# Kernel tuning notes

Measured on AMD Instinct MI355X. Metric: run time of the kernel, lower is better.

Reference implementation:

```python
import jax, jax.numpy as jnp
import numpy as np

SEQ, D_IN, D_OUT = 8192, 768, 768

def setup_inputs() -> dict:
    key = jax.random.key(0)
    k1, k2, k3, k4 = jax.random.split(key, 4)
    scale = 1.0 / np.sqrt(D_IN)
    return {
        "x": jax.random.normal(k1, (SEQ, D_IN), dtype=jnp.float32),
        "w_q": jax.random.normal(k2, (D_OUT, D_IN), dtype=jnp.float32) * scale,
        "w_k": jax.random.normal(k3, (D_OUT, D_IN), dtype=jnp.float32) * scale,
        "w_v": jax.random.normal(k4, (D_OUT, D_IN), dtype=jnp.float32) * scale,
    }

def reference(x, w_q, w_k, w_v):
    # torch Linear: y = x @ W.T (no bias since qkv_bias=False)
    q = x @ w_q.T  # [S, D]
    k = x @ w_k.T  # [S, D]
    v = x @ w_v.T  # [S, D]
    scores = (q @ k.T) / jnp.sqrt(jnp.asarray(k.shape[-1], x.dtype))  # [S, S]
    attn = jax.nn.softmax(scores, axis=-1)
    return attn @ v  # [S, D]
```

## Files before the change

kernel.cpp:

```cpp
#include <hip/hip_runtime.h>

#define SEQ 8192
#define DIM 768

typedef __attribute__((ext_vector_type(8))) short s16x8;
typedef __attribute__((ext_vector_type(4))) float f32x4;

__device__ __forceinline__ unsigned short f2bf(float f) {
  union { float f; unsigned u; } v; v.f = f;
  unsigned r = v.u + 0x7FFFu + ((v.u >> 16) & 1u);
  return (unsigned short)(r >> 16);
}

__device__ __forceinline__ float bf2f(unsigned short s) {
  union { unsigned u; float f; } v; v.u = ((unsigned)s) << 16;
  return v.f;
}

__device__ __forceinline__ void gll16(const void* gsrc, void* ldst) {
  __builtin_amdgcn_global_load_lds(
      (__attribute__((address_space(1))) unsigned int*)gsrc,
      (__attribute__((address_space(3))) unsigned int*)ldst, 16, 0, 0);
}

#define XN4 (SEQ * DIM / 4)
#define WN4 (DIM * DIM / 4)

__global__ void cast_all_kernel(const float* __restrict__ x, const float* __restrict__ wq,
                                const float* __restrict__ wk, const float* __restrict__ wv,
                                unsigned short* __restrict__ dx, unsigned short* __restrict__ dq,
                                unsigned short* __restrict__ dk, unsigned short* __restrict__ dv) {
  int i = blockIdx.x * blockDim.x + threadIdx.x;
  const float* s;
  unsigned short* d;
  int off;
  if (i < XN4) {
    s = x; d = dx; off = i;
  } else {
    int j = i - XN4;
    int wi = j / WN4;
    off = j - wi * WN4;
    s = (wi == 0) ? wq : ((wi == 1) ? wk : wv);
    d = (wi == 0) ? dq : ((wi == 1) ? dk : dv);
  }
  float4 v = ((const float4*)s)[off];
  ushort4 r; r.x = f2bf(v.x); r.y = f2bf(v.y); r.z = f2bf(v.z); r.w = f2bf(v.w);
  ((ushort4*)d)[off] = r;
}

__global__ __launch_bounds__(256, 2)
void proj_kernel(const unsigned short* __restrict__ X,
                 const unsigned short* __restrict__ Wq,
                 const unsigned short* __restrict__ Wk,
                 const unsigned short* __restrict__ Wv,
                 unsigned short* __restrict__ Qb,
                 unsigned short* __restrict__ Kb,
                 unsigned short* __restrict__ Vtb) {
  __shared__ __align__(16) char lds[65536];
  const int tid = threadIdx.x;
  const int lane = tid & 63, wv = tid >> 6;
  const int l15 = lane & 15, l4 = lane >> 4;
  const int mt = blockIdx.x, nt = blockIdx.y, z = blockIdx.z;
  const unsigned short* W = (z == 0) ? Wq : ((z == 1) ? Wk : Wv);

  f32x4 acc[4][4];
#pragma unroll
  for (int i = 0; i < 4; ++i)
#pragma unroll
    for (int j = 0; j < 4; ++j) acc[i][j] = f32x4{0.f, 0.f, 0.f, 0.f};

  auto stage = [&](int kk) {
    char* At = lds + (kk & 1) * 32768;
    char* Bt = At + 16384;
    const int d0 = kk * 64;
#pragma unroll
    for (int i = 0; i < 4; ++i) {
      int s = i * 256 + tid;
      int row = s >> 3, c = (s & 7) ^ (row & 7);
      gll16(X + (long)(mt * 128 + row) * DIM + d0 + c * 8, At + i * 4096 + (wv << 10));
      gll16(W + (long)(nt * 128 + row) * DIM + d0 + c * 8, Bt + i * 4096 + (wv << 10));
    }
  };

  stage(0);
#pragma unroll 1
  for (int kk = 0; kk < 12; ++kk) {
    __syncthreads();
    if (kk + 1 < 12) stage(kk + 1);
    const char* At = lds + (kk & 1) * 32768;
    const char* Bt = At + 16384;
#pragma unroll
    for (int ks = 0; ks < 2; ++ks) {
      const int c = ks * 4 + l4;
      s16x8 a[4], b[4];
#pragma unroll
      for (int mi = 0; mi < 4; ++mi) {
        int row = (wv & 1) * 64 + mi * 16 + l15;
        a[mi] = *(const s16x8*)(At + row * 128 + ((c ^ (row & 7)) << 4));
      }
#pragma unroll
      for (int ni = 0; ni < 4; ++ni) {
        int row = (wv >> 1) * 64 + ni * 16 + l15;
        b[ni] = *(const s16x8*)(Bt + row * 128 + ((c ^ (row & 7)) << 4));
      }
#pragma unroll
      for (int mi = 0; mi < 4; ++mi)
#pragma unroll
        for (int ni = 0; ni < 4; ++ni)
          acc[mi][ni] = __builtin_amdgcn_mfma_f32_16x16x32_bf16(a[mi], b[ni], acc[mi][ni], 0, 0, 0);
    }
  }

#pragma unroll
  for (int mi = 0; mi < 4; ++mi)
#pragma unroll
    for (int ni = 0; ni < 4; ++ni) {
      int row0 = mt * 128 + (wv & 1) * 64 + mi * 16 + l4 * 4;
      int col = nt * 128 + (wv >> 1) * 64 + ni * 16 + l15;
      if (z == 2) {
        ushort4 r;
        r.x = f2bf(acc[mi][ni][0]); r.y = f2bf(acc[mi][ni][1]);
        r.z = f2bf(acc[mi][ni][2]); r.w = f2bf(acc[mi][ni][3]);
        *(ushort4*)(Vtb + (long)(row0 >> 5) * (DIM * 32) + col * 32 + (row0 & 31)) = r;
      } else {
        unsigned short* dst = (z == 0) ? Qb : Kb;
#pragma unroll
        for (int g = 0; g < 4; ++g)
          dst[(long)(row0 + g) * DIM + col] = f2bf(acc[mi][ni][g]);
      }
    }
}

#define SCALE_LOG2E 0.05205878f

__global__ __launch_bounds__(512, 2)
void flash_kernel(const unsigned short* __restrict__ Q,
                  const unsigned short* __restrict__ K,
                  const unsigned short* __restrict__ V,
                  unsigned short* __restrict__ partp,
                  float* __restrict__ outf,
                  float* __restrict__ lout,
                  int kv_len, int norm_out) {
  __shared__ __align__(16) char lds[131072];
  char* Pl = lds + 98304;
  float* l_part = (float*)lds;

  const int tid = threadIdx.x;
  const int lane = tid & 63, wv = tid >> 6;
  const int l15 = lane & 15, l4 = lane >> 4;
  const int qtile = blockIdx.x, split = blockIdx.y;
  const long kv0 = (long)split * kv_len;
  const long qrow0 = (long)qtile * 64;
  const int R = wv & 1;
  const int C = wv >> 1;

  f32x4 acc_o[4][6];
  float acc_lp[8];
#pragma unroll
  for (int i = 0; i < 4; ++i)
#pragma unroll
    for (int j = 0; j < 6; ++j) acc_o[i][j] = f32x4{0.f, 0.f, 0.f, 0.f};
#pragma unroll
  for (int i = 0; i < 8; ++i) acc_lp[i] = 0.f;

  const int niter = kv_len >> 8;

  auto vchunk = [&](int par, int j) -> char* {
    int base = par ? ((j < 5) ? 40960 + j * 8192 : 90112)
                   : ((j < 5) ? j * 8192 : 81920);
    return lds + base;
  };

  auto stageQK = [&](int r, long kbase) {
    char* Qc = lds + (r & 1) * 40960;
    char* Kc = Qc + 8192;
    const int d0 = r * 64;
    {
      int s = tid;
      int row = s >> 3, c = (s & 7) ^ (row & 7);
      gll16(Q + (qrow0 + row) * DIM + d0 + c * 8, Qc + (wv << 10));
    }
#pragma unroll
    for (int i = 0; i < 4; ++i) {
      int s = i * 512 + tid;
      int row = s >> 3, c = (s & 7) ^ (row & 7);
      gll16(K + (kbase + row) * DIM + d0 + c * 8, Kc + i * 8192 + (wv << 10));
    }
  };

  auto stagePV = [&](int v, long kblk0) {
    const int par = v & 1;
    const long blkbase = (kblk0 + v) * (long)(DIM * 32);
    int s = wv * 64 + lane;
    int rp = s >> 3, p3 = s & 7;
    int orig = p3 ^ (rp & 7);
    int vr_in = rp * 2 + (orig >> 2);
    int k4 = orig & 3;
#pragma unroll
    for (int i = 0; i < 6; ++i)
      gll16(V + blkbase + (long)(i * 128 + vr_in) * 32 + k4 * 8, vchunk(par, i) + (wv << 10));
  };

  stageQK(0, kv0);
#pragma unroll 1
  for (int it = 0; it < niter; ++it) {
    const long kb = kv0 + (long)it * 256;
    const long kblk0 = kb >> 5;

    f32x4 acc_s[2][4];
#pragma unroll
    for (int a = 0; a < 2; ++a)
#pragma unroll
      for (int b = 0; b < 4; ++b) acc_s[a][b] = f32x4{0.f, 0.f, 0.f, 0.f};

#pragma unroll 1
    for (int r = 0; r < 12; ++r) {
      __syncthreads();
      if (r + 1 < 12) stageQK(r + 1, kb);
      else stagePV(0, kblk0);
      const char* Qc = lds + (r & 1) * 40960;
      const char* Kc = Qc + 8192;
#pragma unroll
      for (int ks = 0; ks < 2; ++ks) {
        const int c = ks * 4 + l4;
        s16x8 af[2], bk[4];
#pragma unroll
        for (int rt = 0; rt < 2; ++rt) {
          int row = R * 32 + rt * 16 + l15;
          af[rt] = *(const s16x8*)(Qc + row * 128 + ((c ^ (row & 7)) << 4));
        }
#pragma unroll
        for (int ct = 0; ct < 4; ++ct) {
          int kr = C * 64 + ct * 16 + l15;
          bk[ct] = *(const s16x8*)(Kc + kr * 128 + ((c ^ (kr & 7)) << 4));
        }
        __builtin_amdgcn_s_setprio(1);
#pragma unroll
        for (int rt = 0; rt < 2; ++rt)
#pragma unroll
          for (int ct = 0; ct < 4; ++ct)
            acc_s[rt][ct] = __builtin_amdgcn_mfma_f32_16x16x32_bf16(af[rt], bk[ct], acc_s[rt][ct], 0, 0, 0);
        __builtin_amdgcn_s_setprio(0);
      }
    }

#pragma unroll
    for (int rt = 0; rt < 2; ++rt)
#pragma unroll
      for (int ct = 0; ct < 4; ++ct)
#pragma unroll
        for (int g = 0; g < 4; ++g) {
          float p = exp2f(acc_s[rt][ct][g] * SCALE_LOG2E);
          acc_lp[rt * 4 + g] += p;
          int row = R * 32 + rt * 16 + l4 * 4 + g;
          int col = C * 64 + ct * 16 + l15;
          int off = row * 512 + ((((col >> 3) ^ (row & 7))) << 4) + ((col & 7) << 1);
          *(unsigned short*)(Pl + off) = f2bf(p);
        }

#pragma unroll 1
    for (int v = 0; v < 8; ++v) {
      __syncthreads();
      if (v + 1 < 8) stagePV(v + 1, kblk0);
      else if (it + 1 < niter) stageQK(0, kb + 256);
      const int par = v & 1;
      s16x8 pa[4];
      const int ck = v * 4 + l4;
#pragma unroll
      for (int rs = 0; rs < 4; ++rs) {
        int row = rs * 16 + l15;
        int pc = (ck & ~7) | ((ck & 7) ^ (row & 7));
        pa[rs] = *(const s16x8*)(Pl + row * 512 + (pc << 4));
      }
      const int vr_l = wv * 16 + l15;
      const int rp = vr_l >> 1;
      const int p3 = (((l15 & 1) << 2) | l4) ^ (rp & 7);
#pragma unroll
      for (int cc = 0; cc < 3; ++cc)
#pragma unroll
        for (int t = 0; t < 2; ++t) {
          const char* vcb = vchunk(par, cc * 2 + t);
          s16x8 vb = *(const s16x8*)(vcb + rp * 128 + (p3 << 4));
          __builtin_amdgcn_s_setprio(1);
#pragma unroll
          for (int rs = 0; rs < 4; ++rs)
            acc_o[rs][cc * 2 + t] =
                __builtin_amdgcn_mfma_f32_16x16x32_bf16(pa[rs], vb, acc_o[rs][cc * 2 + t], 0, 0, 0);
          __builtin_amdgcn_s_setprio(0);
        }
    }
  }

#pragma unroll
  for (int i = 0; i < 8; ++i) {
    float v = acc_lp[i];
    v += __shfl_xor(v, 1); v += __shfl_xor(v, 2);
    v += __shfl_xor(v, 4); v += __shfl_xor(v, 8);
    acc_lp[i] = v;
  }
  __syncthreads();
  if (l15 == 0) {
#pragma unroll
    for (int rt = 0; rt < 2; ++rt)
#pragma unroll
      for (int g = 0; g < 4; ++g)
        l_part[C * 64 + R * 32 + rt * 16 + l4 * 4 + g] = acc_lp[rt * 4 + g];
  }
  __syncthreads();

  if (!norm_out) {
    if (tid < 64)
      lout[(long)split * SEQ + qrow0 + tid] =
          l_part[tid] + l_part[64 + tid] + l_part[128 + tid] + l_part[192 + tid];
#pragma unroll
    for (int rt = 0; rt < 4; ++rt) {
      int row = rt * 16 + l4 * 4;
#pragma unroll
      for (int j = 0; j < 6; ++j) {
        int cc = j >> 1, t = j & 1;
        int col = (cc * 16 + wv + 8 * t) * 16 + l15;
#pragma unroll
        for (int g = 0; g < 4; ++g)
          partp[(long)split * SEQ * DIM + (qrow0 + row + g) * DIM + col] = f2bf(acc_o[rt][j][g]);
      }
    }
  } else {
    float linv[4][4];
#pragma unroll
    for (int rt = 0; rt < 4; ++rt)
#pragma unroll
      for (int g = 0; g < 4; ++g) {
        int row = rt * 16 + l4 * 4 + g;
        linv[rt][g] = 1.0f / (l_part[row] + l_part[64 + row] + l_part[128 + row] + l_part[192 + row]);
      }
#pragma unroll
    for (int rt = 0; rt < 4; ++rt) {
      int row = rt * 16 + l4 * 4;
#pragma unroll
      for (int j = 0; j < 6; ++j) {
        int cc = j >> 1, t = j & 1;
        int col = (cc * 16 + wv + 8 * t) * 16 + l15;
#pragma unroll
        for (int g = 0; g < 4; ++g)
          outf[(qrow0 + row + g) * DIM + col] = acc_o[rt][j][g] * linv[rt][g];
      }
    }
  }
}

__global__ void combine_kernel(const unsigned short* __restrict__ part,
                               const float* __restrict__ lsum,
                               float* __restrict__ out, int n4) {
  int i = blockIdx.x * blockDim.x + threadIdx.x;
  if (i >= n4) return;
  int row = (i * 4) / DIM;
  ushort4 p0 = ((const ushort4*)part)[i];
  ushort4 p1 = ((const ushort4*)(part + (long)SEQ * DIM))[i];
  float inv = 1.0f / (lsum[row] + lsum[SEQ + row]);
  float4 o;
  o.x = (bf2f(p0.x) + bf2f(p1.x)) * inv;
  o.y = (bf2f(p0.y) + bf2f(p1.y)) * inv;
  o.z = (bf2f(p0.z) + bf2f(p1.z)) * inv;
  o.w = (bf2f(p0.w) + bf2f(p1.w)) * inv;
  ((float4*)out)[i] = o;
}

extern "C" void kernel_launch(void* const* d_in, const int* in_sizes, int n_in,
                              void* d_out, int out_size, void* d_ws, size_t ws_size,
                              hipStream_t stream) {
  const float* x = (const float*)d_in[0];
  const float* wq = (const float*)d_in[1];
  const float* wk = (const float*)d_in[2];
  const float* wv = (const float*)d_in[3];
  float* out = (float*)d_out;
  char* ws = (char*)d_ws;

  const size_t o_xbf = 0;
  const size_t o_wq = o_xbf + (size_t)SEQ * DIM * 2;
  const size_t o_wk = o_wq + (size_t)DIM * DIM * 2;
  const size_t o_wv = o_wk + (size_t)DIM * DIM * 2;
  const size_t o_q = o_wv + (size_t)DIM * DIM * 2;
  const size_t o_k = o_q + (size_t)SEQ * DIM * 2;
  const size_t o_vt = o_k + (size_t)SEQ * DIM * 2;
  const size_t o_part = o_vt + (size_t)SEQ * DIM * 2;
  const size_t o_l = o_part + (size_t)2 * SEQ * DIM * 2;
  const size_t total_g2 = o_l + (size_t)2 * SEQ * 4;

  unsigned short* Xbf = (unsigned short*)(ws + o_xbf);
  unsigned short* Wqb = (unsigned short*)(ws + o_wq);
  unsigned short* Wkb = (unsigned short*)(ws + o_wk);
  unsigned short* Wvb = (unsigned short*)(ws + o_wv);
  unsigned short* Qb = (unsigned short*)(ws + o_q);
  unsigned short* Kb = (unsigned short*)(ws + o_k);
  unsigned short* Vtb = (unsigned short*)(ws + o_vt);
  unsigned short* part = (unsigned short*)(ws + o_part);
  float* lbuf = (float*)(ws + o_l);

  const int G = (ws_size >= total_g2) ? 2 : 1;

  cast_all_kernel<<<7872, 256, 0, stream>>>(x, wq, wk, wv, Xbf, Wqb, Wkb, Wvb);
  proj_kernel<<<dim3(64, 6, 3), 256, 0, stream>>>(Xbf, Wqb, Wkb, Wvb, Qb, Kb, Vtb);
  if (G == 2) {
    flash_kernel<<<dim3(128, 2), 512, 0, stream>>>(Qb, Kb, Vtb, part, nullptr, lbuf, SEQ / 2, 0);
    combine_kernel<<<6144, 256, 0, stream>>>(part, lbuf, out, SEQ * DIM / 4);
  } else {
    flash_kernel<<<dim3(128, 1), 512, 0, stream>>>(Qb, Kb, Vtb, nullptr, out, nullptr, SEQ, 1);
  }
}
```

Baseline: 315.9 us.

## Load V fragments directly from global into registers, removing PV LDS staging

The PV phase no longer stages V blocks through LDS with async global-to-LDS copies and per-chunk barriers. Each wave now loads its V fragments straight into registers from the pre-tiled V layout, double-buffered across the eight chunks. The next Q/K stage is prefetched at the end of the QK loop instead. This removes eight barriers per iteration and shrinks LDS, at the cost of more vector registers and exposed global load latency inside the MFMA loop.

```diff
diff --git a/kernel.cpp b/kernel.cpp
--- a/kernel.cpp
+++ b/kernel.cpp
@@ -133,6 +133,35 @@
 
 #define SCALE_LOG2E 0.05205878f
 
+#define LOADVB(arr, vv)                                                            \
+  do {                                                                             \
+    const unsigned short* Vb_ = V + (long)(kblk0 + (vv)) * (DIM * 32);             \
+    _Pragma("unroll")                                                              \
+    for (int j_ = 0; j_ < 6; ++j_)                                                 \
+      arr[j_] = *(const s16x8*)(Vb_ + (j_ * 128 + wv * 16 + l15) * 32 + l4 * 8);   \
+  } while (0)
+
+#define PVCHUNK(vv, CUR, NXT)                                                      \
+  do {                                                                             \
+    if ((vv) + 1 < 8) LOADVB(NXT, (vv) + 1);                                       \
+    s16x8 pa_[4];                                                                  \
+    const int ck_ = (vv) * 4 + l4;                                                 \
+    _Pragma("unroll")                                                              \
+    for (int rs_ = 0; rs_ < 4; ++rs_) {                                            \
+      int row_ = rs_ * 16 + l15;                                                   \
+      int pc_ = (ck_ & ~7) | ((ck_ & 7) ^ (row_ & 7));                             \
+      pa_[rs_] = *(const s16x8*)(Pl + row_ * 512 + (pc_ << 4));                    \
+    }                                                                              \
+    __builtin_amdgcn_s_setprio(1);                                                 \
+    _Pragma("unroll")                                                              \
+    for (int j_ = 0; j_ < 6; ++j_)                                                 \
+      _Pragma("unroll")                                                            \
+      for (int rs_ = 0; rs_ < 4; ++rs_)                                            \
+        acc_o[rs_][j_] =                                                           \
+            __builtin_amdgcn_mfma_f32_16x16x32_bf16(pa_[rs_], CUR[j_], acc_o[rs_][j_], 0, 0, 0); \
+    __builtin_amdgcn_s_setprio(0);                                                 \
+  } while (0)
+
 __global__ __launch_bounds__(512, 2)
 void flash_kernel(const unsigned short* __restrict__ Q,
                   const unsigned short* __restrict__ K,
@@ -141,8 +170,8 @@
                   float* __restrict__ outf,
                   float* __restrict__ lout,
                   int kv_len, int norm_out) {
-  __shared__ __align__(16) char lds[131072];
-  char* Pl = lds + 98304;
+  __shared__ __align__(16) char lds[114688];
+  char* Pl = lds + 81920;
   float* l_part = (float*)lds;
 
   const int tid = threadIdx.x;
@@ -165,12 +194,6 @@
 
   const int niter = kv_len >> 8;
 
-  auto vchunk = [&](int par, int j) -> char* {
-    int base = par ? ((j < 5) ? 40960 + j * 8192 : 90112)
-                   : ((j < 5) ? j * 8192 : 81920);
-    return lds + base;
-  };
-
   auto stageQK = [&](int r, long kbase) {
     char* Qc = lds + (r & 1) * 40960;
     char* Kc = Qc + 8192;
@@ -188,19 +211,6 @@
     }
   };
 
-  auto stagePV = [&](int v, long kblk0) {
-    const int par = v & 1;
-    const long blkbase = (kblk0 + v) * (long)(DIM * 32);
-    int s = wv * 64 + lane;
-    int rp = s >> 3, p3 = s & 7;
-    int orig = p3 ^ (rp & 7);
-    int vr_in = rp * 2 + (orig >> 2);
-    int k4 = orig & 3;
-#pragma unroll
-    for (int i = 0; i < 6; ++i)
-      gll16(V + blkbase + (long)(i * 128 + vr_in) * 32 + k4 * 8, vchunk(par, i) + (wv << 10));
-  };
-
   stageQK(0, kv0);
 #pragma unroll 1
   for (int it = 0; it < niter; ++it) {
@@ -217,7 +227,7 @@
     for (int r = 0; r < 12; ++r) {
       __syncthreads();
       if (r + 1 < 12) stageQK(r + 1, kb);
-      else stagePV(0, kblk0);
+      else if (it + 1 < niter) stageQK(0, kb + 256);
       const char* Qc = lds + (r & 1) * 40960;
       const char* Kc = Qc + 8192;
 #pragma unroll
@@ -243,6 +253,9 @@
         __builtin_amdgcn_s_setprio(0);
       }
     }
+
+    s16x8 vbA[6], vbB[6];
+    LOADVB(vbA, 0);
 
 #pragma unroll
     for (int rt = 0; rt < 2; ++rt)
@@ -257,38 +270,16 @@
           int off = row * 512 + ((((col >> 3) ^ (row & 7))) << 4) + ((col & 7) << 1);
           *(unsigned short*)(Pl + off) = f2bf(p);
         }
-
-#pragma unroll 1
-    for (int v = 0; v < 8; ++v) {
-      __syncthreads();
-      if (v + 1 < 8) stagePV(v + 1, kblk0);
-      else if (it + 1 < niter) stageQK(0, kb + 256);
-      const int par = v & 1;
-      s16x8 pa[4];
-      const int ck = v * 4 + l4;
-#pragma unroll
-      for (int rs = 0; rs < 4; ++rs) {
-        int row = rs * 16 + l15;
-        int pc = (ck & ~7) | ((ck & 7) ^ (row & 7));
-        pa[rs] = *(const s16x8*)(Pl + row * 512 + (pc << 4));
-      }
-      const int vr_l = wv * 16 + l15;
-      const int rp = vr_l >> 1;
-      const int p3 = (((l15 & 1) << 2) | l4) ^ (rp & 7);
-#pragma unroll
-      for (int cc = 0; cc < 3; ++cc)
-#pragma unroll
-        for (int t = 0; t < 2; ++t) {
-          const char* vcb = vchunk(par, cc * 2 + t);
-          s16x8 vb = *(const s16x8*)(vcb + rp * 128 + (p3 << 4));
-          __builtin_amdgcn_s_setprio(1);
-#pragma unroll
-          for (int rs = 0; rs < 4; ++rs)
-            acc_o[rs][cc * 2 + t] =
-                __builtin_amdgcn_mfma_f32_16x16x32_bf16(pa[rs], vb, acc_o[rs][cc * 2 + t], 0, 0, 0);
-          __builtin_amdgcn_s_setprio(0);
-        }
-    }
+    __syncthreads();
+
+    PVCHUNK(0, vbA, vbB);
+    PVCHUNK(1, vbB, vbA);
+    PVCHUNK(2, vbA, vbB);
+    PVCHUNK(3, vbB, vbA);
+    PVCHUNK(4, vbA, vbB);
+    PVCHUNK(5, vbB, vbA);
+    PVCHUNK(6, vbA, vbB);
+    PVCHUNK(7, vbB, vbA);
   }
 
 #pragma unroll
```

Result: faster. 301.4 us (median of 2 runs) (-4.6%).
